# Kernel optimization log

Measured on AMD Instinct MI355X. Metric: run time of the kernel, lower is better.

The kernel has to match this reference:

```python
import jax, jax.numpy as jnp
import numpy as np

K = 6                 # color-coding parameter; K-1 message-passing steps
N = 50000             # num nodes
E = 1600000           # num edges (avg degree 32)
F = 384               # num_node_features = K * 2**K


def setup_inputs() -> dict:
    key = jax.random.key(0)
    k1, k2, k3, k4, k5 = jax.random.split(key, 5)
    s = 1.0 / np.sqrt(F)
    x = jax.random.normal(k1, (N, F), dtype=jnp.float32)
    edge_index = jax.random.randint(k2, (2, E), 0, N, dtype=jnp.int32)
    batch = jnp.zeros((N,), dtype=jnp.int32)  # unused by forward, kept for signature parity
    W_rel = jax.random.normal(k3, (F, F), dtype=jnp.float32) * s   # GraphConv lin_rel weight
    W_root = jax.random.normal(k4, (F, F), dtype=jnp.float32) * s  # GraphConv lin_root weight
    W_lin = jax.random.normal(k5, (1, F), dtype=jnp.float32) * s   # readout linear (no bias)
    return {"x": x, "edge_index": edge_index, "batch": batch,
            "W_rel": W_rel, "W_root": W_root, "W_lin": W_lin}


def reference(x, edge_index, batch, W_rel, W_root, W_lin):
    src = edge_index[0]
    dst = edge_index[1]
    # K-1 iterations of PyG GraphConv(aggr='add', bias=False) + relu:
    #   out = segment_sum(x[src] -> dst) @ W_rel^T + x @ W_root^T
    for _ in range(K - 1):
        agg = jax.ops.segment_sum(x[src], dst, num_segments=N)  # [N, F]
        x = jax.nn.relu(agg @ W_rel.T + x @ W_root.T)
    # readout: Linear(F, 1, bias=False)
    return x @ W_lin.T  # [N, 1]
```

## Files before the change

### kernel.cpp

```cpp
#include <hip/hip_runtime.h>
#include <hip/hip_bf16.h>

#define NN 50000
#define EE 1600000
#define FF 384
#define MPAD 50048
#define NITER 5
#define EPB 6250
#define BCAP 220000

typedef unsigned int u32;
typedef unsigned short u16;
typedef __attribute__((ext_vector_type(8))) short short8;
typedef __attribute__((ext_vector_type(4))) float f32x4;

typedef const __attribute__((address_space(1))) void* gptr_t;
typedef __attribute__((address_space(3))) void* lptr_t;

__device__ __forceinline__ float bf_lo(u32 u) {
  u32 v = u << 16;
  return __builtin_bit_cast(float, v);
}
__device__ __forceinline__ float bf_hi(u32 u) {
  u32 v = u & 0xFFFF0000u;
  return __builtin_bit_cast(float, v);
}
__device__ __forceinline__ u32 f2bf(float f) {
  u32 u = __builtin_bit_cast(u32, f);
  return (u + 0x7FFFu + ((u >> 16) & 1u)) >> 16;
}
__device__ __forceinline__ u32 pack2(float lo, float hi) {
  return f2bf(lo) | (f2bf(hi) << 16);
}
__device__ __forceinline__ void load16_lds(const void* g, void* l) {
  __builtin_amdgcn_global_load_lds((gptr_t)g, (lptr_t)l, 16, 0, 0);
}

__global__ void hist_kernel(const int* __restrict__ key, int* __restrict__ cnt) {
  int e = blockIdx.x * 256 + threadIdx.x;
  if (e < EE) atomicAdd(&cnt[key[e]], 1);
}

__global__ void scan_kernel(const int* __restrict__ cnt, int* __restrict__ row_start,
                            int* __restrict__ cursor, int* __restrict__ bcur) {
  __shared__ int wsum[4];
  const int CH = 196;
  int t = threadIdx.x;
  if (t < 8) bcur[t] = t * BCAP;
  int lo = t * CH;
  int hi = lo + CH; if (hi > NN) hi = NN;
  int s = 0;
  int n4 = (hi - lo) >> 2;
  const int4* p = (const int4*)(cnt + lo);
  for (int i = 0; i < n4; ++i) { int4 c = p[i]; s += c.x + c.y + c.z + c.w; }
  int lane = t & 63, w = t >> 6;
  int v = s;
  for (int d = 1; d < 64; d <<= 1) { int u = __shfl_up(v, d, 64); if (lane >= d) v += u; }
  if (lane == 63) wsum[w] = v;
  __syncthreads();
  int run = v - s;
  for (int i = 0; i < w; ++i) run += wsum[i];
  int4* q1 = (int4*)(row_start + lo);
  int4* q2 = (int4*)(cursor + lo);
  for (int k = 0; k < n4; ++k) {
    int4 c = p[k];
    int4 o; o.x = run; o.y = run + c.x; o.z = o.y + c.y; o.w = o.z + c.z;
    run = o.w + c.w;
    q1[k] = o; q2[k] = o;
  }
  if (hi == NN && lo < NN) row_start[NN] = run;
}

__global__ __launch_bounds__(256) void bucket_scatter_kernel(
    const int* __restrict__ src, const int* __restrict__ dst,
    int* __restrict__ bcur, int* __restrict__ es_src, int* __restrict__ es_dst) {
  __shared__ int osrc[EPB];
  __shared__ int odst[EPB];
  __shared__ int h[8], lo8[8], gbase[8], c2[8];
  const int t = threadIdx.x;
  if (t < 8) { h[t] = 0; c2[t] = 0; }
  __syncthreads();
  const int e0 = blockIdx.x * EPB;
  for (int i = t; i < EPB; i += 256) {
    int d = dst[e0 + i];
    atomicAdd(&h[d / 6250], 1);
  }
  __syncthreads();
  if (t == 0) { int r = 0; for (int b = 0; b < 8; ++b) { lo8[b] = r; r += h[b]; } }
  __syncthreads();
  if (t < 8) gbase[t] = atomicAdd(&bcur[t], h[t]);
  __syncthreads();
  for (int i = t; i < EPB; i += 256) {
    int s = src[e0 + i], d = dst[e0 + i];
    int b = d / 6250;
    int p = lo8[b] + atomicAdd(&c2[b], 1);
    osrc[p] = s; odst[p] = d;
  }
  __syncthreads();
  for (int i = t; i < EPB; i += 256) {
    int b = 0;
    while (b < 7 && i >= lo8[b + 1]) ++b;
    int g = gbase[b] + (i - lo8[b]);
    es_src[g] = osrc[i];
    es_dst[g] = odst[i];
  }
}

__global__ void scatter_final_kernel(const int* __restrict__ es_src,
                                     const int* __restrict__ es_dst,
                                     const int* __restrict__ bcur,
                                     int* __restrict__ cursor, int* __restrict__ col) {
  const int g = blockIdx.x & 7;
  const int bi = blockIdx.x >> 3;
  const int base = g * BCAP;
  const int cnt = bcur[g] - base;
  for (int i = bi * 256 + threadIdx.x; i < cnt; i += 64 * 256) {
    int d = es_dst[base + i];
    int p = atomicAdd(&cursor[d], 1);
    col[p] = es_src[base + i];
  }
}

__global__ void convert_x_kernel(const float* __restrict__ xin, u16* __restrict__ xout) {
  size_t i = ((size_t)blockIdx.x * 256 + threadIdx.x) * 4;
  if (i >= (size_t)NN * FF) return;
  float4 f = *(const float4*)(xin + i);
  u32 o0 = pack2(f.x, f.y);
  u32 o1 = pack2(f.z, f.w);
  u32* q = (u32*)(xout + i);
  q[0] = o0; q[1] = o1;
}

__global__ void build_bt_kernel(const float* __restrict__ Wr, const float* __restrict__ Wt,
                                u16* __restrict__ Bt) {
  int i = blockIdx.x * 256 + threadIdx.x;
  if (i >= FF * 2 * FF) return;
  int n = i / (2 * FF);
  int k = i - n * (2 * FF);
  float v = (k < FF) ? Wr[n * FF + k] : Wt[n * FF + (k - FF)];
  Bt[i] = (u16)f2bf(v);
}

__global__ void spmm_pass_kernel(const u16* __restrict__ x, const int* __restrict__ rs,
                                 const int* __restrict__ col, u16* __restrict__ agg,
                                 const int fo) {
  int row = blockIdx.x * 4 + (threadIdx.x >> 6);
  int lane = threadIdx.x & 63;
  if (row >= NN) return;
  int j0 = rs[row], j1 = rs[row + 1];
  float alo = 0.f, ahi = 0.f;
  const u32* xw = (const u32*)x + fo + lane;
  int j = j0;
  for (; j + 8 <= j1; j += 8) {
    int s0 = col[j + 0], s1 = col[j + 1], s2 = col[j + 2], s3 = col[j + 3];
    int s4 = col[j + 4], s5 = col[j + 5], s6 = col[j + 6], s7 = col[j + 7];
    u32 u0 = xw[(size_t)s0 * 192];
    u32 u1 = xw[(size_t)s1 * 192];
    u32 u2 = xw[(size_t)s2 * 192];
    u32 u3 = xw[(size_t)s3 * 192];
    u32 u4 = xw[(size_t)s4 * 192];
    u32 u5 = xw[(size_t)s5 * 192];
    u32 u6 = xw[(size_t)s6 * 192];
    u32 u7 = xw[(size_t)s7 * 192];
    alo += bf_lo(u0) + bf_lo(u1) + bf_lo(u2) + bf_lo(u3) +
           bf_lo(u4) + bf_lo(u5) + bf_lo(u6) + bf_lo(u7);
    ahi += bf_hi(u0) + bf_hi(u1) + bf_hi(u2) + bf_hi(u3) +
           bf_hi(u4) + bf_hi(u5) + bf_hi(u6) + bf_hi(u7);
  }
  for (; j < j1; ++j) {
    u32 u = xw[(size_t)col[j] * 192];
    alo += bf_lo(u); ahi += bf_hi(u);
  }
  ((u32*)agg)[(size_t)row * 192 + fo + lane] = pack2(alo, ahi);
}

__global__ __launch_bounds__(512, 4) void gemm_kernel(
    const u16* __restrict__ Aagg, const u16* __restrict__ Ax,
    const u16* __restrict__ Bt, u16* __restrict__ Xout) {
  __shared__ __align__(16) u16 As[2][64 * 64];
  __shared__ __align__(16) u16 Bs[384 * 64];

  const int orig = blockIdx.x;
  const int xcd = orig & 7, idx = orig >> 3;
  const int wg = ((xcd < 6) ? xcd * 98 : 6 * 98 + (xcd - 6) * 97) + idx;
  const int m0 = wg * 64;

  const int tid = threadIdx.x;
  const int lane = tid & 63;
  const int w = tid >> 6;
  const int wr = w >> 2;
  const int wc = w & 3;

  f32x4 acc[2][6] = {};

#define STAGE_A(KT, BUF)                                                        \
  {                                                                             \
    const u16* Asrc_ = ((KT) < 6) ? Aagg : Ax;                                  \
    const int kbA_ = (((KT) < 6) ? (KT) : (KT)-6) << 7;                         \
    const int rA_ = tid >> 3;                                                   \
    const int bcA_ = (tid & 7) << 4;                                            \
    load16_lds((const char*)Asrc_ + (size_t)(m0 + rA_) * 768 + kbA_ +           \
                   (bcA_ ^ ((rA_ & 7) << 4)),                                   \
               (char*)&As[BUF][0] + tid * 16);                                  \
  }

#define STAGE_B(KT)                                                             \
  {                                                                             \
    const int kbB_ = (KT) << 7;                                                 \
    _Pragma("unroll")                                                           \
    for (int i = 0; i < 6; ++i) {                                               \
      const int c = tid + i * 512;                                              \
      const int rB_ = c >> 3;                                                   \
      const int bcB_ = (c & 7) << 4;                                            \
      load16_lds((const char*)Bt + (size_t)rB_ * 1536 + kbB_ +                  \
                     (bcB_ ^ ((rB_ & 7) << 4)),                                 \
                 (char*)&Bs[0] + c * 16);                                       \
    }                                                                           \
  }

  STAGE_A(0, 0);
  STAGE_B(0);
  __syncthreads();

  int buf = 0;
  for (int kt = 0; kt < 12; ++kt) {
    if (kt < 11) STAGE_A(kt + 1, buf ^ 1);
#pragma unroll
    for (int ks = 0; ks < 2; ++ks) {
      short8 af[2], bfm[6];
#pragma unroll
      for (int ni = 0; ni < 6; ++ni) {
        const int r = wc * 96 + ni * 16 + (lane & 15);
        const int bc = (ks * 64 + ((lane >> 4) << 4)) ^ ((r & 7) << 4);
        bfm[ni] = *(const short8*)((const char*)&Bs[0] + r * 128 + bc);
      }
#pragma unroll
      for (int mi = 0; mi < 2; ++mi) {
        const int r = wr * 32 + mi * 16 + (lane & 15);
        const int bc = (ks * 64 + ((lane >> 4) << 4)) ^ ((r & 7) << 4);
        af[mi] = *(const short8*)((const char*)&As[buf][0] + r * 128 + bc);
      }
#pragma unroll
      for (int mi = 0; mi < 2; ++mi)
#pragma unroll
        for (int ni = 0; ni < 6; ++ni)
          acc[mi][ni] = __builtin_amdgcn_mfma_f32_16x16x32_bf16(af[mi], bfm[ni], acc[mi][ni], 0, 0, 0);
    }
    __syncthreads();
    if (kt < 11) {
      STAGE_B(kt + 1);
      __syncthreads();
    }
    buf ^= 1;
  }

#pragma unroll
  for (int mi = 0; mi < 2; ++mi) {
#pragma unroll
    for (int r = 0; r < 4; ++r) {
      const int row = m0 + wr * 32 + mi * 16 + ((lane >> 4) << 2) + r;
      u16* orow = Xout + (size_t)row * FF + wc * 96 + (lane & 15);
#pragma unroll
      for (int ni = 0; ni < 6; ++ni) {
        float v = fmaxf(acc[mi][ni][r], 0.0f);
        orow[ni * 16] = (u16)f2bf(v);
      }
    }
  }
#undef STAGE_A
#undef STAGE_B
}

__global__ void readout_kernel(const u16* __restrict__ x, const float* __restrict__ wl,
                               float* __restrict__ out) {
  int row = blockIdx.x * 4 + (threadIdx.x >> 6);
  int lane = threadIdx.x & 63;
  if (row >= NN) return;
  const u32* p = (const u32*)(x + (size_t)row * FF) + lane * 3;
  u32 u0 = p[0], u1 = p[1], u2 = p[2];
  const float* w = wl + lane * 6;
  float s = bf_lo(u0) * w[0] + bf_hi(u0) * w[1] +
            bf_lo(u1) * w[2] + bf_hi(u1) * w[3] +
            bf_lo(u2) * w[4] + bf_hi(u2) * w[5];
#pragma unroll
  for (int off = 32; off > 0; off >>= 1) s += __shfl_down(s, off, 64);
  if (lane == 0) out[row] = s;
}

extern "C" void kernel_launch(void* const* d_in, const int* in_sizes, int n_in,
                              void* d_out, int out_size, void* d_ws, size_t ws_size,
                              hipStream_t stream) {
  const float* x_in = (const float*)d_in[0];
  const int* ei = (const int*)d_in[1];
  const float* W_rel = (const float*)d_in[3];
  const float* W_root = (const float*)d_in[4];
  const float* W_lin = (const float*)d_in[5];
  float* out = (float*)d_out;

  char* ws = (char*)d_ws;
  int* cnt = (int*)(ws);
  int* bcur = cnt + NN;
  int* row_start = (int*)(ws + 200064);
  int* cursor = (int*)(ws + 400128);
  int* col = (int*)(ws + 600192);
  u16* Bt = (u16*)(ws + 7000192);
  u16* agg = (u16*)(ws + 7590016);
  u16* x0 = (u16*)(ws + 46026880);
  u16* x1 = (u16*)(ws + 84463744);
  if (ws_size < (size_t)122900608) return;
  int* es_src = (int*)(ws + 7590016);
  int* es_dst = (int*)(ws + 7590016 + 7040000);

  const int* esrc = ei;
  const int* edst = ei + EE;

  hipMemsetAsync(cnt, 0, NN * sizeof(int), stream);
  hipMemsetAsync(agg + (size_t)NN * FF, 0, (size_t)(MPAD - NN) * FF * sizeof(u16), stream);
  hipMemsetAsync(x0 + (size_t)NN * FF, 0, (size_t)(MPAD - NN) * FF * sizeof(u16), stream);
  hipMemsetAsync(x1 + (size_t)NN * FF, 0, (size_t)(MPAD - NN) * FF * sizeof(u16), stream);

  hist_kernel<<<EE / 256, 256, 0, stream>>>(edst, cnt);
  scan_kernel<<<1, 256, 0, stream>>>(cnt, row_start, cursor, bcur);
  bucket_scatter_kernel<<<EE / EPB, 256, 0, stream>>>(esrc, edst, bcur, es_src, es_dst);
  scatter_final_kernel<<<512, 256, 0, stream>>>(es_src, es_dst, bcur, cursor, col);
  convert_x_kernel<<<(NN * FF / 4 + 255) / 256, 256, 0, stream>>>(x_in, x0);
  build_bt_kernel<<<(FF * 2 * FF + 255) / 256, 256, 0, stream>>>(W_rel, W_root, Bt);

  u16* xs = x0;
  u16* xd = x1;
  for (int t = 0; t < NITER; ++t) {
    for (int p = 0; p < 3; ++p)
      spmm_pass_kernel<<<NN / 4, 256, 0, stream>>>(xs, row_start, col, agg, p * 64);
    gemm_kernel<<<MPAD / 64, 512, 0, stream>>>(agg, xs, Bt, xd);
    u16* tmp = xs; xs = xd; xd = tmp;
  }
  readout_kernel<<<NN / 4, 256, 0, stream>>>(xs, W_lin, out);
}
```

Before: 1.240 ms.

## Rebuild CSR with per-bucket LDS histograms and fuse SpMM passes into one launch

CSR construction now buckets edges first, then builds per-bucket histograms and scatter cursors in shared memory using only 8 blocks. This replaces global atomics over all nodes and drops the cnt memset and cursor copy. The SpMM now uses 16-lane groups per row covering 16 word-columns, with 12 passes folded into a single launch. Column indices are loaded cooperatively and broadcast by shuffle, with nontemporal loads and stores. The 8-block CSR kernels have very low parallelism, and the narrower feature slices mean each gathered row is revisited across 12 passes, which may hurt cache locality.

```diff
diff --git a/kernel.cpp b/kernel.cpp
--- a/kernel.cpp
+++ b/kernel.cpp
@@ -8,6 +8,10 @@
 #define NITER 5
 #define EPB 6250
 #define BCAP 220000
+#define GRP 6250
+#define RPB 16
+#define RBLK 3125
+#define NPASS 12
 
 typedef unsigned int u32;
 typedef unsigned short u16;
@@ -36,17 +40,65 @@
   __builtin_amdgcn_global_load_lds((gptr_t)g, (lptr_t)l, 16, 0, 0);
 }
 
-__global__ void hist_kernel(const int* __restrict__ key, int* __restrict__ cnt) {
-  int e = blockIdx.x * 256 + threadIdx.x;
-  if (e < EE) atomicAdd(&cnt[key[e]], 1);
-}
-
-__global__ void scan_kernel(const int* __restrict__ cnt, int* __restrict__ row_start,
-                            int* __restrict__ cursor, int* __restrict__ bcur) {
+__global__ void init_bcur_kernel(int* __restrict__ bcur) {
+  if (threadIdx.x < 8) bcur[threadIdx.x] = threadIdx.x * BCAP;
+}
+
+__global__ __launch_bounds__(256) void bucket_scatter_kernel(
+    const int* __restrict__ src, const int* __restrict__ dst,
+    int* __restrict__ bcur, int* __restrict__ es_src, int* __restrict__ es_dst) {
+  __shared__ int osrc[EPB];
+  __shared__ int odst[EPB];
+  __shared__ int h[8], lo8[8], gbase[8], c2[8];
+  const int t = threadIdx.x;
+  if (t < 8) { h[t] = 0; c2[t] = 0; }
+  __syncthreads();
+  const int e0 = blockIdx.x * EPB;
+  for (int i = t; i < EPB; i += 256) {
+    int d = dst[e0 + i];
+    atomicAdd(&h[d / GRP], 1);
+  }
+  __syncthreads();
+  if (t == 0) { int r = 0; for (int b = 0; b < 8; ++b) { lo8[b] = r; r += h[b]; } }
+  __syncthreads();
+  if (t < 8) gbase[t] = atomicAdd(&bcur[t], h[t]);
+  __syncthreads();
+  for (int i = t; i < EPB; i += 256) {
+    int s = src[e0 + i], d = dst[e0 + i];
+    int b = d / GRP;
+    int p = lo8[b] + atomicAdd(&c2[b], 1);
+    osrc[p] = s; odst[p] = d;
+  }
+  __syncthreads();
+  for (int i = t; i < EPB; i += 256) {
+    int b = 0;
+    while (b < 7 && i >= lo8[b + 1]) ++b;
+    int g = gbase[b] + (i - lo8[b]);
+    es_src[g] = osrc[i];
+    es_dst[g] = odst[i];
+  }
+}
+
+__global__ __launch_bounds__(512) void hist2_kernel(
+    const int* __restrict__ es_dst, const int* __restrict__ bcur,
+    int* __restrict__ cnt) {
+  __shared__ int h[GRP];
+  const int g = blockIdx.x;
+  const int lo = g * GRP;
+  const int base = g * BCAP;
+  const int n = bcur[g] - base;
+  for (int i = threadIdx.x; i < GRP; i += 512) h[i] = 0;
+  __syncthreads();
+  for (int i = threadIdx.x; i < n; i += 512)
+    atomicAdd(&h[es_dst[base + i] - lo], 1);
+  __syncthreads();
+  for (int i = threadIdx.x; i < GRP; i += 512) cnt[lo + i] = h[i];
+}
+
+__global__ void scan_kernel(const int* __restrict__ cnt, int* __restrict__ row_start) {
   __shared__ int wsum[4];
   const int CH = 196;
   int t = threadIdx.x;
-  if (t < 8) bcur[t] = t * BCAP;
   int lo = t * CH;
   int hi = lo + CH; if (hi > NN) hi = NN;
   int s = 0;
@@ -61,63 +113,31 @@
   int run = v - s;
   for (int i = 0; i < w; ++i) run += wsum[i];
   int4* q1 = (int4*)(row_start + lo);
-  int4* q2 = (int4*)(cursor + lo);
   for (int k = 0; k < n4; ++k) {
     int4 c = p[k];
     int4 o; o.x = run; o.y = run + c.x; o.z = o.y + c.y; o.w = o.z + c.z;
     run = o.w + c.w;
-    q1[k] = o; q2[k] = o;
+    q1[k] = o;
   }
   if (hi == NN && lo < NN) row_start[NN] = run;
 }
 
-__global__ __launch_bounds__(256) void bucket_scatter_kernel(
-    const int* __restrict__ src, const int* __restrict__ dst,
-    int* __restrict__ bcur, int* __restrict__ es_src, int* __restrict__ es_dst) {
-  __shared__ int osrc[EPB];
-  __shared__ int odst[EPB];
-  __shared__ int h[8], lo8[8], gbase[8], c2[8];
-  const int t = threadIdx.x;
-  if (t < 8) { h[t] = 0; c2[t] = 0; }
-  __syncthreads();
-  const int e0 = blockIdx.x * EPB;
-  for (int i = t; i < EPB; i += 256) {
-    int d = dst[e0 + i];
-    atomicAdd(&h[d / 6250], 1);
-  }
-  __syncthreads();
-  if (t == 0) { int r = 0; for (int b = 0; b < 8; ++b) { lo8[b] = r; r += h[b]; } }
-  __syncthreads();
-  if (t < 8) gbase[t] = atomicAdd(&bcur[t], h[t]);
-  __syncthreads();
-  for (int i = t; i < EPB; i += 256) {
-    int s = src[e0 + i], d = dst[e0 + i];
-    int b = d / 6250;
-    int p = lo8[b] + atomicAdd(&c2[b], 1);
-    osrc[p] = s; odst[p] = d;
-  }
-  __syncthreads();
-  for (int i = t; i < EPB; i += 256) {
-    int b = 0;
-    while (b < 7 && i >= lo8[b + 1]) ++b;
-    int g = gbase[b] + (i - lo8[b]);
-    es_src[g] = osrc[i];
-    es_dst[g] = odst[i];
-  }
-}
-
-__global__ void scatter_final_kernel(const int* __restrict__ es_src,
-                                     const int* __restrict__ es_dst,
-                                     const int* __restrict__ bcur,
-                                     int* __restrict__ cursor, int* __restrict__ col) {
-  const int g = blockIdx.x & 7;
-  const int bi = blockIdx.x >> 3;
+__global__ __launch_bounds__(512) void scatter2_kernel(
+    const int* __restrict__ es_src, const int* __restrict__ es_dst,
+    const int* __restrict__ bcur, const int* __restrict__ row_start,
+    int* __restrict__ col) {
+  __shared__ int cur[GRP];
+  const int g = blockIdx.x;
+  const int lo = g * GRP;
   const int base = g * BCAP;
-  const int cnt = bcur[g] - base;
-  for (int i = bi * 256 + threadIdx.x; i < cnt; i += 64 * 256) {
+  const int n = bcur[g] - base;
+  for (int i = threadIdx.x; i < GRP; i += 512) cur[i] = row_start[lo + i];
+  __syncthreads();
+  for (int i = threadIdx.x; i < n; i += 512) {
     int d = es_dst[base + i];
-    int p = atomicAdd(&cursor[d], 1);
-    col[p] = es_src[base + i];
+    int s = es_src[base + i];
+    int p = atomicAdd(&cur[d - lo], 1);
+    col[p] = s;
   }
 }
 
@@ -141,37 +161,41 @@
   Bt[i] = (u16)f2bf(v);
 }
 
-__global__ void spmm_pass_kernel(const u16* __restrict__ x, const int* __restrict__ rs,
-                                 const int* __restrict__ col, u16* __restrict__ agg,
-                                 const int fo) {
-  int row = blockIdx.x * 4 + (threadIdx.x >> 6);
-  int lane = threadIdx.x & 63;
-  if (row >= NN) return;
-  int j0 = rs[row], j1 = rs[row + 1];
+__global__ __launch_bounds__(256) void spmm12_kernel(
+    const u16* __restrict__ x, const int* __restrict__ rs,
+    const int* __restrict__ col, u16* __restrict__ agg) {
+  const int pass = blockIdx.x / RBLK;
+  const int rb = blockIdx.x - pass * RBLK;
+  const int lane = threadIdx.x & 63;
+  const int sl = lane & 15;
+  const int r = rb * RPB + (threadIdx.x >> 6) * 4 + (lane >> 4);
+  const int fo = pass * 16;
+
+  const int j0 = rs[r], j1 = rs[r + 1];
+  const u32* xw = (const u32*)x + fo + sl;
   float alo = 0.f, ahi = 0.f;
-  const u32* xw = (const u32*)x + fo + lane;
+
   int j = j0;
-  for (; j + 8 <= j1; j += 8) {
-    int s0 = col[j + 0], s1 = col[j + 1], s2 = col[j + 2], s3 = col[j + 3];
-    int s4 = col[j + 4], s5 = col[j + 5], s6 = col[j + 6], s7 = col[j + 7];
-    u32 u0 = xw[(size_t)s0 * 192];
-    u32 u1 = xw[(size_t)s1 * 192];
-    u32 u2 = xw[(size_t)s2 * 192];
-    u32 u3 = xw[(size_t)s3 * 192];
-    u32 u4 = xw[(size_t)s4 * 192];
-    u32 u5 = xw[(size_t)s5 * 192];
-    u32 u6 = xw[(size_t)s6 * 192];
-    u32 u7 = xw[(size_t)s7 * 192];
-    alo += bf_lo(u0) + bf_lo(u1) + bf_lo(u2) + bf_lo(u3) +
-           bf_lo(u4) + bf_lo(u5) + bf_lo(u6) + bf_lo(u7);
-    ahi += bf_hi(u0) + bf_hi(u1) + bf_hi(u2) + bf_hi(u3) +
-           bf_hi(u4) + bf_hi(u5) + bf_hi(u6) + bf_hi(u7);
-  }
-  for (; j < j1; ++j) {
-    u32 u = xw[(size_t)col[j] * 192];
-    alo += bf_lo(u); ahi += bf_hi(u);
-  }
-  ((u32*)agg)[(size_t)row * 192 + fo + lane] = pack2(alo, ahi);
+  for (; j + 16 <= j1; j += 16) {
+    int colv = __builtin_nontemporal_load(col + j + sl);
+#pragma unroll
+    for (int k = 0; k < 16; ++k) {
+      int s = __shfl(colv, k, 16);
+      u32 u = xw[(size_t)s * 192];
+      alo += bf_lo(u); ahi += bf_hi(u);
+    }
+  }
+  if (j < j1) {
+    int idx = j + sl; if (idx >= j1) idx = j1 - 1;
+    int colv = __builtin_nontemporal_load(col + idx);
+    int n = j1 - j;
+    for (int k = 0; k < n; ++k) {
+      int s = __shfl(colv, k, 16);
+      u32 u = xw[(size_t)s * 192];
+      alo += bf_lo(u); ahi += bf_hi(u);
+    }
+  }
+  __builtin_nontemporal_store(pack2(alo, ahi), (u32*)agg + (size_t)r * 192 + fo + sl);
 }
 
 __global__ __launch_bounds__(512, 4) void gemm_kernel(
@@ -301,7 +325,6 @@
   int* cnt = (int*)(ws);
   int* bcur = cnt + NN;
   int* row_start = (int*)(ws + 200064);
-  int* cursor = (int*)(ws + 400128);
   int* col = (int*)(ws + 600192);
   u16* Bt = (u16*)(ws + 7000192);
   u16* agg = (u16*)(ws + 7590016);
@@ -314,23 +337,22 @@
   const int* esrc = ei;
   const int* edst = ei + EE;
 
-  hipMemsetAsync(cnt, 0, NN * sizeof(int), stream);
   hipMemsetAsync(agg + (size_t)NN * FF, 0, (size_t)(MPAD - NN) * FF * sizeof(u16), stream);
   hipMemsetAsync(x0 + (size_t)NN * FF, 0, (size_t)(MPAD - NN) * FF * sizeof(u16), stream);
   hipMemsetAsync(x1 + (size_t)NN * FF, 0, (size_t)(MPAD - NN) * FF * sizeof(u16), stream);
 
-  hist_kernel<<<EE / 256, 256, 0, stream>>>(edst, cnt);
-  scan_kernel<<<1, 256, 0, stream>>>(cnt, row_start, cursor, bcur);
+  init_bcur_kernel<<<1, 64, 0, stream>>>(bcur);
   bucket_scatter_kernel<<<EE / EPB, 256, 0, stream>>>(esrc, edst, bcur, es_src, es_dst);
-  scatter_final_kernel<<<512, 256, 0, stream>>>(es_src, es_dst, bcur, cursor, col);
+  hist2_kernel<<<8, 512, 0, stream>>>(es_dst, bcur, cnt);
+  scan_kernel<<<1, 256, 0, stream>>>(cnt, row_start);
+  scatter2_kernel<<<8, 512, 0, stream>>>(es_src, es_dst, bcur, row_start, col);
   convert_x_kernel<<<(NN * FF / 4 + 255) / 256, 256, 0, stream>>>(x_in, x0);
   build_bt_kernel<<<(FF * 2 * FF + 255) / 256, 256, 0, stream>>>(W_rel, W_root, Bt);
 
   u16* xs = x0;
   u16* xd = x1;
   for (int t = 0; t < NITER; ++t) {
-    for (int p = 0; p < 3; ++p)
-      spmm_pass_kernel<<<NN / 4, 256, 0, stream>>>(xs, row_start, col, agg, p * 64);
+    spmm12_kernel<<<NPASS * RBLK, 256, 0, stream>>>(xs, row_start, col, agg);
     gemm_kernel<<<MPAD / 64, 512, 0, stream>>>(agg, xs, Bt, xd);
     u16* tmp = xs; xs = xd; xd = tmp;
   }
```

Measured after the change: 1.917 ms. 1.55x slower.
